# Optimization experiments

Measured on AMD Instinct MI355X. Metric: run time of the kernel, lower is better.

The kernel has to match this reference:

```python
import jax, jax.numpy as jnp
import numpy as np

NUM_HIDDENS = 1024
NUM_VOCABS = 4096
BATCH = 64
SEQ = 256


def setup_inputs() -> dict:
    key = jax.random.key(0)
    ks = jax.random.split(key, 16)
    V, H = NUM_VOCABS, NUM_HIDDENS

    def gate(k1, k2):
        return (jax.random.normal(k1, (V, H), jnp.float32) * 0.01,
                jax.random.normal(k2, (H, H), jnp.float32) * 0.01,
                jnp.zeros((H,), jnp.float32))

    f_w_xh, f_w_hh, f_b = gate(ks[0], ks[1])
    i_w_xh, i_w_hh, i_b = gate(ks[2], ks[3])
    c_w_xh, c_w_hh, c_b = gate(ks[4], ks[5])
    o_w_xh, o_w_hh, o_b = gate(ks[6], ks[7])
    y_w_ho = jax.random.normal(ks[8], (H, V), jnp.float32) * 0.01
    y_b_o = jnp.zeros((V,), jnp.float32)
    inputs = jax.random.randint(ks[9], (BATCH, SEQ), 0, V, dtype=jnp.int64)
    H0 = jnp.zeros((BATCH, H), jnp.float32)
    C0 = jnp.zeros((BATCH, H), jnp.float32)
    return dict(inputs=inputs, H0=H0, C0=C0,
                f_w_xh=f_w_xh, f_w_hh=f_w_hh, f_b=f_b,
                i_w_xh=i_w_xh, i_w_hh=i_w_hh, i_b=i_b,
                c_w_xh=c_w_xh, c_w_hh=c_w_hh, c_b=c_b,
                o_w_xh=o_w_xh, o_w_hh=o_w_hh, o_b=o_b,
                y_w_ho=y_w_ho, y_b_o=y_b_o)


def reference(inputs, H0, C0,
              f_w_xh, f_w_hh, f_b,
              i_w_xh, i_w_hh, i_b,
              c_w_xh, c_w_hh, c_b,
              o_w_xh, o_w_hh, o_b,
              y_w_ho, y_b_o):
    # inputs: (batch, seq) int tokens -> iterate over time (seq, batch)
    tokens = inputs.T  # (T, B)

    def step(carry, x_t):
        Hs, Cs = carry
        # one_hot(x) @ W_xh == gather of rows: exact same math in fp32
        f = jax.nn.sigmoid(f_w_xh[x_t] + Hs @ f_w_hh + f_b)
        i = jax.nn.sigmoid(i_w_xh[x_t] + Hs @ i_w_hh + i_b)
        o = jax.nn.sigmoid(o_w_xh[x_t] + Hs @ o_w_hh + o_b)
        C_tilde = jnp.tanh(c_w_xh[x_t] + Hs @ c_w_hh + c_b)
        Cn = f * Cs + i * C_tilde
        Hn = o * Cn  # NOTE: source applies no tanh here (faithful)
        Y = Hn @ y_w_ho + y_b_o
        return (Hn, Cn), Y

    (Hf, Cf), Ys = jax.lax.scan(step, (H0, C0), tokens)
    return Ys, Hf, Cf  # Ys: (T, B, V)
```

## Files before the change

### kernel.cpp

```cpp
#include <hip/hip_runtime.h>
#include <stdint.h>
#include <stddef.h>


#define B_ 64
#define H_ 1024
#define V_ 4096
#define T_ 256
#define NWG 128

typedef __attribute__((ext_vector_type(8))) short short8;
typedef __attribute__((ext_vector_type(4))) float f32x4;
typedef __attribute__((ext_vector_type(4))) float float4_;
typedef __attribute__((ext_vector_type(4))) unsigned int uint4v;

static __device__ __forceinline__ unsigned short f2bf(float f) {
  union { float f; unsigned int u; } v; v.f = f;
  unsigned int u = v.u;
  unsigned int r = (u + 0x7fffu + ((u >> 16) & 1u)) >> 16;
  return (unsigned short)r;
}

static __device__ __forceinline__ void gload_lds16(const void* g, void* l) {
  __builtin_amdgcn_global_load_lds((const __attribute__((address_space(1))) unsigned int*)g,
                                   (__attribute__((address_space(3))) unsigned int*)l,
                                   16, 0, 0);
}

static __device__ __forceinline__ void sc_store_u32(unsigned int* p, unsigned int v) {
  asm volatile("global_store_dword %0, %1, off sc0 sc1"
               :: "v"((unsigned long long)p), "v"(v) : "memory");
}

static __device__ __forceinline__ void pollw(const unsigned int* arr, unsigned int tgt, int lane) {
  const unsigned long long a0 = (unsigned long long)arr + (unsigned long long)lane * 16;
  const unsigned long long a1 = a0 + 1024;
  while (true) {
    uint4v v0, v1;
    asm volatile("global_load_dwordx4 %0, %2, off sc0 sc1\n\t"
                 "global_load_dwordx4 %1, %3, off sc0 sc1\n\t"
                 "s_waitcnt vmcnt(0)"
                 : "=&v"(v0), "=&v"(v1) : "v"(a0), "v"(a1) : "memory");
    const bool ok = v0[0] >= tgt && v0[1] >= tgt && v0[2] >= tgt && v0[3] >= tgt &&
                    v1[0] >= tgt && v1[1] >= tgt && v1[2] >= tgt && v1[3] >= tgt;
    if (__all(ok)) break;
  }
  asm volatile("" ::: "memory");
  __builtin_amdgcn_sched_barrier(0);
}

__global__ void transpose_bf16_kernel(const float* __restrict__ src, int src_cols,
                                      unsigned short* __restrict__ dst,
                                      int c_mul, int c_add) {
  __shared__ float tile[64][65];
  const int k0 = blockIdx.x * 64, h0 = blockIdx.y * 64;
  const int t = threadIdx.x;
  {
    const int kk = t >> 2, seg = (t & 3) * 16;
    const float* s = src + (size_t)(k0 + kk) * src_cols + h0 + seg;
#pragma unroll
    for (int j = 0; j < 16; j += 4) {
      float4_ v = *(const float4_*)(s + j);
      tile[kk][seg + j + 0] = v[0];
      tile[kk][seg + j + 1] = v[1];
      tile[kk][seg + j + 2] = v[2];
      tile[kk][seg + j + 3] = v[3];
    }
  }
  __syncthreads();
  {
    const int hh = t >> 2, ks = (t & 3) * 16;
    const int c = (h0 + hh) * c_mul + c_add;
    short8 p0, p1;
#pragma unroll
    for (int j = 0; j < 8; ++j) {
      p0[j] = (short)f2bf(tile[ks + j][hh]);
      p1[j] = (short)f2bf(tile[ks + 8 + j][hh]);
    }
    unsigned short* d = dst + (size_t)c * 1024 + k0 + ks;
    *(short8*)(d) = p0;
    *(short8*)(d + 8) = p1;
  }
}

__global__ void init_kernel(const float* __restrict__ H0,
                            unsigned short* __restrict__ Hbuf0,
                            unsigned int* __restrict__ arr) {
  const int i = blockIdx.x * 256 + threadIdx.x;
  Hbuf0[i] = f2bf(H0[i]);
  if (i < 512) sc_store_u32(arr + i, 0u);
}

#define AOFF 65536

__launch_bounds__(256, 1)
__global__ void lstm_persistent_kernel(
    const unsigned short* __restrict__ Wcat,
    unsigned short* __restrict__ Hbuf,
    unsigned int* __restrict__ arr,
    const float* __restrict__ C0,
    const float* __restrict__ xwf, const float* __restrict__ xwi,
    const float* __restrict__ xwc, const float* __restrict__ xwo,
    const float* __restrict__ bfv, const float* __restrict__ biv,
    const float* __restrict__ bcv, const float* __restrict__ bov,
    const int* __restrict__ tokens,
    float* __restrict__ outH, float* __restrict__ outC) {
  __shared__ __align__(16) unsigned char lds[147456];
  const int tid = threadIdx.x;
  const int wave = tid >> 6, lane = tid & 63;
  const int l15 = lane & 15, l4 = lane >> 4;
  const int wgc0 = blockIdx.x * 32;
  const int hbase0 = wgc0 >> 2;
  const int brow = wave * 16 + l15;
  unsigned int* myslot = arr + blockIdx.x * 4 + wave;

  auto xw_of = [&](int g) -> const float* {
    return g == 0 ? xwf : g == 1 ? xwi : g == 2 ? xwc : xwo;
  };
  auto b_of = [&](int g) -> const float* {
    return g == 0 ? bfv : g == 1 ? biv : g == 2 ? bcv : bov;
  };

  int hL[2];
  float bias8[2][4], Creg[2], xg[2][4], xgn[2][4];
#pragma unroll
  for (int ni = 0; ni < 2; ++ni) {
    hL[ni] = hbase0 + ni * 4 + l4;
#pragma unroll
    for (int r = 0; r < 4; ++r) bias8[ni][r] = b_of(r)[hL[ni]];
    Creg[ni] = C0[(size_t)brow * 1024 + hL[ni]];
  }
  {
    const int tk = tokens[brow * T_ + 0];
#pragma unroll
    for (int ni = 0; ni < 2; ++ni)
#pragma unroll
      for (int r = 0; r < 4; ++r)
        xg[ni][r] = xw_of(r)[(size_t)tk * 1024 + hL[ni]];
  }

  {
    const char* Wb = (const char*)(Wcat + (size_t)wgc0 * 1024);
#pragma unroll
    for (int it = 0; it < 16; ++it) {
      const int D = it * 4096 + wave * 1024 + lane * 16;
      const int row = D >> 11, off = D & 2047;
      const int so = off ^ ((row & 7) << 4);
      gload_lds16(Wb + (size_t)row * 2048 + so, &lds[it * 4096 + wave * 1024]);
    }
  }
  asm volatile("s_waitcnt vmcnt(0)" ::: "memory");
  __syncthreads();

  auto stageA = [&](int buf, int c, const char* Hsrc) {
#pragma unroll
    for (int it2 = 0; it2 < 4; ++it2) {
      const int row = wave * 16 + it2 * 4 + l4;
      const int so = (l15 * 16) ^ ((row & 7) << 4);
      gload_lds16(Hsrc + (size_t)row * 2048 + c * 256 + so,
                  &lds[AOFF + buf * 16384 + wave * 4096 + it2 * 1024]);
    }
  };

  const int bswz = (l15 & 7) << 4;
  f32x4 acc[2];
  const f32x4 zz = {0.f, 0.f, 0.f, 0.f};

#pragma unroll 1
  for (int t = 0; t < T_; ++t) {
    if (t > 0) pollw(arr, (unsigned int)t, lane);

    const char* Hs = (const char*)(Hbuf + (size_t)t * 65536);
    stageA(0, 0, Hs);
    stageA(1, 1, Hs);
    stageA(2, 2, Hs);
    stageA(3, 3, Hs);

    __builtin_amdgcn_sched_barrier(0);
    int tok2 = tokens[brow * T_ + ((t + 1) & (T_ - 1))];
    __builtin_amdgcn_sched_barrier(0);

    acc[0] = zz; acc[1] = zz;
#pragma unroll
    for (int c = 0; c < 8; ++c) {
      if (c < 4)       asm volatile("s_waitcnt vmcnt(13)" ::: "memory");
      else if (c == 4) asm volatile("s_waitcnt vmcnt(12)" ::: "memory");
      else if (c == 5) asm volatile("s_waitcnt vmcnt(8)" ::: "memory");
      else if (c == 6) asm volatile("s_waitcnt vmcnt(4)" ::: "memory");
      else             asm volatile("s_waitcnt vmcnt(0)" ::: "memory");
      __builtin_amdgcn_sched_barrier(0);
      if (c < 4) stageA((c + 4) % 5, c + 4, Hs);
      __builtin_amdgcn_sched_barrier(0);
      {
        const int abase = AOFF + (c % 5) * 16384;
        const int abyte = abase + brow * 256;
        const int aswz = (brow & 7) << 4;
#pragma unroll
        for (int ks = 0; ks < 4; ++ks) {
          const int koff = ks * 64 + l4 * 16;
          short8 a  = *(const short8*)&lds[abyte + (koff ^ aswz)];
          short8 b0 = *(const short8*)&lds[(size_t)l15 * 2048 + ((c * 256 + koff) ^ bswz)];
          short8 b1 = *(const short8*)&lds[(size_t)(16 + l15) * 2048 + ((c * 256 + koff) ^ bswz)];
          acc[0] = __builtin_amdgcn_mfma_f32_16x16x32_bf16(b0, a, acc[0], 0, 0, 0);
          acc[1] = __builtin_amdgcn_mfma_f32_16x16x32_bf16(b1, a, acc[1], 0, 0, 0);
        }
      }
      __builtin_amdgcn_sched_barrier(0);
    }

    if (t > 0) {
#pragma unroll
      for (int ni = 0; ni < 2; ++ni)
#pragma unroll
        for (int r = 0; r < 4; ++r) xg[ni][r] = xgn[ni][r];
    }

    unsigned short* Hout = Hbuf + (size_t)(t + 1) * 65536;
    unsigned int dat32[2][2];
#pragma unroll
    for (int ni = 0; ni < 2; ++ni) {
      const f32x4 v = acc[ni];
      const float pre0 = v[0] + xg[ni][0] + bias8[ni][0];
      const float pre1 = v[1] + xg[ni][1] + bias8[ni][1];
      const float pre2 = v[2] + xg[ni][2] + bias8[ni][2];
      const float pre3 = v[3] + xg[ni][3] + bias8[ni][3];
      const float pf = 1.f / (1.f + __expf(-pre0));
      const float pi = 1.f / (1.f + __expf(-pre1));
      const float e2 = __expf(2.f * pre2);
      const float pc = (e2 - 1.f) / (e2 + 1.f);
      const float po = 1.f / (1.f + __expf(-pre3));
      const float cn = pf * Creg[ni] + pi * pc;
      Creg[ni] = cn;
      const float hv = po * cn;
      const unsigned int sbf = f2bf(hv);
      const unsigned int p = sbf | (((unsigned int)__shfl_down(sbf, 16)) << 16);
      dat32[ni][0] = p;
      dat32[ni][1] = __shfl_down(p, 32);
      if (t == T_ - 1) {
        const size_t idx = (size_t)brow * 1024 + hL[ni];
        outH[idx] = hv; outC[idx] = cn;
      }
    }
    if (l4 == 0) {
      uint4v dat;
      dat.x = dat32[0][0]; dat.y = dat32[0][1];
      dat.z = dat32[1][0]; dat.w = dat32[1][1];
      const unsigned long long addr =
          (unsigned long long)(Hout + (size_t)brow * 1024 + hbase0);
      asm volatile("global_store_dwordx4 %0, %1, off sc0 sc1"
                   :: "v"(addr), "v"(dat) : "memory");
    }

    if (t < T_ - 1) {
      asm volatile("s_waitcnt vmcnt(0)" ::: "memory");
      if (lane == 0) sc_store_u32(myslot, (unsigned int)(t + 1));

#pragma unroll
      for (int ni = 0; ni < 2; ++ni)
#pragma unroll
        for (int r = 0; r < 4; ++r)
          xgn[ni][r] = xw_of(r)[(size_t)tok2 * 1024 + hL[ni]];
    }
  }
}

__launch_bounds__(256, 1)
__global__ void out_gemm_kernel(const unsigned short* __restrict__ A,
                                const unsigned short* __restrict__ Bw,
                                const float* __restrict__ bias,
                                float* __restrict__ Yout) {
  __shared__ unsigned char Ash[2][8192];
  __shared__ unsigned char Bsh[2][8192];
  const int tid = threadIdx.x;
  const int wave = tid >> 6, lane = tid & 63;
  const int wm = wave >> 1, wn = wave & 1;
  const int bid = blockIdx.x;
  const int tn = bid & 31, tm = bid >> 5;

  const char* Agb = (const char*)(A + (size_t)tm * 128 * 1024);
  const char* Bgb = (const char*)(Bw + (size_t)tn * 128 * 1024);

  f32x4 acc[4][4];
  const f32x4 zz = {0.f, 0.f, 0.f, 0.f};
#pragma unroll
  for (int mi = 0; mi < 4; ++mi)
#pragma unroll
    for (int ni = 0; ni < 4; ++ni) acc[mi][ni] = zz;

  auto stage = [&](int buf, int kc) {
#pragma unroll
    for (int j = 0; j < 2; ++j) {
      const int wbase = wave * 2048 + j * 1024;
      const int D = wbase + lane * 16;
      const int row = D >> 6, off = D & 63;
      const int so = off ^ ((row & 3) << 4);
      gload_lds16(Agb + (size_t)row * 2048 + kc * 64 + so, &Ash[buf][wbase]);
      gload_lds16(Bgb + (size_t)row * 2048 + kc * 64 + so, &Bsh[buf][wbase]);
    }
  };

  stage(0, 0);
  __syncthreads();

#pragma unroll 1
  for (int kc = 0; kc < 32; ++kc) {
    const int cur = kc & 1;
    if (kc < 31) stage(cur ^ 1, kc + 1);
    short8 a[4], b[4];
#pragma unroll
    for (int mi = 0; mi < 4; ++mi) {
      const int row = wm * 64 + mi * 16 + (lane & 15);
      const int off = ((lane >> 4) * 16) ^ ((row & 3) << 4);
      a[mi] = *(const short8*)&Ash[cur][row * 64 + off];
    }
#pragma unroll
    for (int ni = 0; ni < 4; ++ni) {
      const int row = wn * 64 + ni * 16 + (lane & 15);
      const int off = ((lane >> 4) * 16) ^ ((row & 3) << 4);
      b[ni] = *(const short8*)&Bsh[cur][row * 64 + off];
    }
#pragma unroll
    for (int mi = 0; mi < 4; ++mi)
#pragma unroll
      for (int ni = 0; ni < 4; ++ni)
        acc[mi][ni] = __builtin_amdgcn_mfma_f32_16x16x32_bf16(a[mi], b[ni], acc[mi][ni], 0, 0, 0);
    __syncthreads();
  }

  const int l15 = lane & 15, l4 = lane >> 4;
#pragma unroll
  for (int ni = 0; ni < 4; ++ni) {
    const int n = tn * 128 + wn * 64 + ni * 16 + l15;
    const float bv = bias[n];
#pragma unroll
    for (int mi = 0; mi < 4; ++mi) {
#pragma unroll
      for (int r = 0; r < 4; ++r) {
        const int m = tm * 128 + wm * 64 + mi * 16 + l4 * 4 + r;
        Yout[(size_t)m * 4096 + n] = acc[mi][ni][r] + bv;
      }
    }
  }
}

extern "C" void kernel_launch(void* const* d_in, const int* in_sizes, int n_in,
                              void* d_out, int out_size, void* d_ws, size_t ws_size,
                              hipStream_t stream) {
  const int* tokens   = (const int*)d_in[0];
  const float* H0     = (const float*)d_in[1];
  const float* C0     = (const float*)d_in[2];
  const float* f_w_xh = (const float*)d_in[3];
  const float* f_w_hh = (const float*)d_in[4];
  const float* f_b    = (const float*)d_in[5];
  const float* i_w_xh = (const float*)d_in[6];
  const float* i_w_hh = (const float*)d_in[7];
  const float* i_b    = (const float*)d_in[8];
  const float* c_w_xh = (const float*)d_in[9];
  const float* c_w_hh = (const float*)d_in[10];
  const float* c_b    = (const float*)d_in[11];
  const float* o_w_xh = (const float*)d_in[12];
  const float* o_w_hh = (const float*)d_in[13];
  const float* o_b    = (const float*)d_in[14];
  const float* y_w_ho = (const float*)d_in[15];
  const float* y_b_o  = (const float*)d_in[16];

  char* ws = (char*)d_ws;
  unsigned short* Wcat = (unsigned short*)ws;
  unsigned short* ywT  = (unsigned short*)(ws + (size_t)(8u << 20));
  unsigned short* Hbuf = (unsigned short*)(ws + (size_t)(16u << 20));
  unsigned int* arr = (unsigned int*)(ws + (size_t)(16u << 20) + (size_t)257 * 65536 * 2);
  const size_t needed = (size_t)(16u << 20) + (size_t)257 * 65536 * 2 + 2048;
  if (ws_size < needed) return;

  const dim3 thr(256);
  hipLaunchKernelGGL(transpose_bf16_kernel, dim3(16, 16), thr, 0, stream, f_w_hh, 1024, Wcat, 4, 0);
  hipLaunchKernelGGL(transpose_bf16_kernel, dim3(16, 16), thr, 0, stream, i_w_hh, 1024, Wcat, 4, 1);
  hipLaunchKernelGGL(transpose_bf16_kernel, dim3(16, 16), thr, 0, stream, c_w_hh, 1024, Wcat, 4, 2);
  hipLaunchKernelGGL(transpose_bf16_kernel, dim3(16, 16), thr, 0, stream, o_w_hh, 1024, Wcat, 4, 3);
  hipLaunchKernelGGL(transpose_bf16_kernel, dim3(16, 64), thr, 0, stream, y_w_ho, 4096, ywT, 1, 0);
  hipLaunchKernelGGL(init_kernel, dim3(256), thr, 0, stream, H0, Hbuf, arr);

  float* outH = (float*)d_out + (size_t)T_ * B_ * V_;
  hipLaunchKernelGGL(lstm_persistent_kernel, dim3(NWG), thr, 0, stream,
                     Wcat, Hbuf, arr, C0,
                     f_w_xh, i_w_xh, c_w_xh, o_w_xh,
                     f_b, i_b, c_b, o_b,
                     tokens, outH, outH + 65536);

  hipLaunchKernelGGL(out_gemm_kernel, dim3(4096), thr, 0, stream,
                     Hbuf + 65536, ywT, y_b_o, (float*)d_out);
}
```

Before: 1.347 ms.

## Shrink barrier flags to u16, pipeline polling, fuse prep kernels, swizzle GEMM blocks

Sync flags shrink from 32-bit to 16-bit so one dwordx4 load per lane covers all 512 flags, and the poll loop keeps a second load in flight while it checks the first. The x-gather loads move to just after staging the H tile so they overlap the recurrent matmul (vmcnt thresholds adjusted). Five transpose launches and the init launch are merged into one prep kernel, and the output GEMM block order is remapped for better cache locality. Together these target barrier latency in the serial timestep loop and launch overhead, with the risk of extra outstanding-load pressure and a wrong vmcnt count.

```diff
diff --git a/kernel.cpp b/kernel.cpp
--- a/kernel.cpp
+++ b/kernel.cpp
@@ -27,34 +27,62 @@
                                    16, 0, 0);
 }
 
-static __device__ __forceinline__ void sc_store_u32(unsigned int* p, unsigned int v) {
-  asm volatile("global_store_dword %0, %1, off sc0 sc1"
+static __device__ __forceinline__ void sc_store_u16(unsigned short* p, unsigned int v) {
+  asm volatile("global_store_short %0, %1, off sc0 sc1"
                :: "v"((unsigned long long)p), "v"(v) : "memory");
 }
 
-static __device__ __forceinline__ void pollw(const unsigned int* arr, unsigned int tgt, int lane) {
-  const unsigned long long a0 = (unsigned long long)arr + (unsigned long long)lane * 16;
-  const unsigned long long a1 = a0 + 1024;
+static __device__ __forceinline__ bool ok8(const uint4v& v, unsigned int tgt) {
+  return (v[0] & 0xffffu) >= tgt && (v[0] >> 16) >= tgt &&
+         (v[1] & 0xffffu) >= tgt && (v[1] >> 16) >= tgt &&
+         (v[2] & 0xffffu) >= tgt && (v[2] >> 16) >= tgt &&
+         (v[3] & 0xffffu) >= tgt && (v[3] >> 16) >= tgt;
+}
+
+static __device__ __forceinline__ void pollw16(const unsigned short* arr, unsigned int tgt,
+                                               int lane, uint4v& v0, uint4v& v1) {
+  const unsigned long long a = (unsigned long long)arr + (unsigned long long)lane * 16u;
+  asm volatile("global_load_dwordx4 %0, %1, off sc0 sc1" : "=&v"(v0) : "v"(a) : "memory");
   while (true) {
-    uint4v v0, v1;
-    asm volatile("global_load_dwordx4 %0, %2, off sc0 sc1\n\t"
-                 "global_load_dwordx4 %1, %3, off sc0 sc1\n\t"
-                 "s_waitcnt vmcnt(0)"
-                 : "=&v"(v0), "=&v"(v1) : "v"(a0), "v"(a1) : "memory");
-    const bool ok = v0[0] >= tgt && v0[1] >= tgt && v0[2] >= tgt && v0[3] >= tgt &&
-                    v1[0] >= tgt && v1[1] >= tgt && v1[2] >= tgt && v1[3] >= tgt;
-    if (__all(ok)) break;
+    asm volatile("global_load_dwordx4 %0, %1, off sc0 sc1\n\ts_waitcnt vmcnt(1)"
+                 : "=&v"(v1) : "v"(a) : "memory");
+    if (__all(ok8(v0, tgt))) break;
+    asm volatile("global_load_dwordx4 %0, %1, off sc0 sc1\n\ts_waitcnt vmcnt(1)"
+                 : "=&v"(v0) : "v"(a) : "memory");
+    if (__all(ok8(v1, tgt))) break;
   }
   asm volatile("" ::: "memory");
   __builtin_amdgcn_sched_barrier(0);
 }
 
-__global__ void transpose_bf16_kernel(const float* __restrict__ src, int src_cols,
-                                      unsigned short* __restrict__ dst,
-                                      int c_mul, int c_add) {
+__global__ void prep_kernel(const float* __restrict__ f_w_hh, const float* __restrict__ i_w_hh,
+                            const float* __restrict__ c_w_hh, const float* __restrict__ o_w_hh,
+                            const float* __restrict__ y_w_ho,
+                            unsigned short* __restrict__ Wcat, unsigned short* __restrict__ ywT,
+                            const float* __restrict__ H0, unsigned short* __restrict__ Hbuf0,
+                            unsigned short* __restrict__ arr) {
+  const int z = blockIdx.z;
+  const int t = threadIdx.x;
+  if (z == 5) {
+    const int b = blockIdx.y * 16 + blockIdx.x;
+    if (b < 256) {
+      const int i = b * 256 + t;
+      Hbuf0[i] = f2bf(H0[i]);
+    } else if (b == 256 && t < 512) {
+      sc_store_u16(arr + t, 0u);
+    }
+    return;
+  }
+  const float* src; unsigned short* dst; int src_cols, c_mul, c_add;
+  if (z < 4) {
+    if (blockIdx.y >= 16) return;
+    src = (z == 0) ? f_w_hh : (z == 1) ? i_w_hh : (z == 2) ? c_w_hh : o_w_hh;
+    dst = Wcat; src_cols = 1024; c_mul = 4; c_add = z;
+  } else {
+    src = y_w_ho; dst = ywT; src_cols = 4096; c_mul = 1; c_add = 0;
+  }
   __shared__ float tile[64][65];
   const int k0 = blockIdx.x * 64, h0 = blockIdx.y * 64;
-  const int t = threadIdx.x;
   {
     const int kk = t >> 2, seg = (t & 3) * 16;
     const float* s = src + (size_t)(k0 + kk) * src_cols + h0 + seg;
@@ -83,21 +111,13 @@
   }
 }
 
-__global__ void init_kernel(const float* __restrict__ H0,
-                            unsigned short* __restrict__ Hbuf0,
-                            unsigned int* __restrict__ arr) {
-  const int i = blockIdx.x * 256 + threadIdx.x;
-  Hbuf0[i] = f2bf(H0[i]);
-  if (i < 512) sc_store_u32(arr + i, 0u);
-}
-
 #define AOFF 65536
 
 __launch_bounds__(256, 1)
 __global__ void lstm_persistent_kernel(
     const unsigned short* __restrict__ Wcat,
     unsigned short* __restrict__ Hbuf,
-    unsigned int* __restrict__ arr,
+    unsigned short* __restrict__ arr,
     const float* __restrict__ C0,
     const float* __restrict__ xwf, const float* __restrict__ xwi,
     const float* __restrict__ xwc, const float* __restrict__ xwo,
@@ -112,7 +132,7 @@
   const int wgc0 = blockIdx.x * 32;
   const int hbase0 = wgc0 >> 2;
   const int brow = wave * 16 + l15;
-  unsigned int* myslot = arr + blockIdx.x * 4 + wave;
+  unsigned short* myslot = arr + blockIdx.x * 4 + wave;
 
   auto xw_of = [&](int g) -> const float* {
     return g == 0 ? xwf : g == 1 ? xwi : g == 2 ? xwc : xwo;
@@ -122,7 +142,7 @@
   };
 
   int hL[2];
-  float bias8[2][4], Creg[2], xg[2][4], xgn[2][4];
+  float bias8[2][4], Creg[2], xg[2][4];
 #pragma unroll
   for (int ni = 0; ni < 2; ++ni) {
     hL[ni] = hbase0 + ni * 4 + l4;
@@ -130,14 +150,7 @@
     for (int r = 0; r < 4; ++r) bias8[ni][r] = b_of(r)[hL[ni]];
     Creg[ni] = C0[(size_t)brow * 1024 + hL[ni]];
   }
-  {
-    const int tk = tokens[brow * T_ + 0];
-#pragma unroll
-    for (int ni = 0; ni < 2; ++ni)
-#pragma unroll
-      for (int r = 0; r < 4; ++r)
-        xg[ni][r] = xw_of(r)[(size_t)tk * 1024 + hL[ni]];
-  }
+  int tok2 = tokens[brow * T_ + 0];
 
   {
     const char* Wb = (const char*)(Wcat + (size_t)wgc0 * 1024);
@@ -165,25 +178,31 @@
   const int bswz = (l15 & 7) << 4;
   f32x4 acc[2];
   const f32x4 zz = {0.f, 0.f, 0.f, 0.f};
+  uint4v pk0 = {0, 0, 0, 0}, pk1 = {0, 0, 0, 0};
 
 #pragma unroll 1
   for (int t = 0; t < T_; ++t) {
-    if (t > 0) pollw(arr, (unsigned int)t, lane);
+    pollw16(arr, (unsigned int)t, lane, pk0, pk1);
 
     const char* Hs = (const char*)(Hbuf + (size_t)t * 65536);
     stageA(0, 0, Hs);
     stageA(1, 1, Hs);
     stageA(2, 2, Hs);
     stageA(3, 3, Hs);
-
     __builtin_amdgcn_sched_barrier(0);
-    int tok2 = tokens[brow * T_ + ((t + 1) & (T_ - 1))];
+    const int tok_next = tokens[brow * T_ + ((t + 1) & (T_ - 1))];
     __builtin_amdgcn_sched_barrier(0);
+#pragma unroll
+    for (int ni = 0; ni < 2; ++ni)
+#pragma unroll
+      for (int r = 0; r < 4; ++r)
+        xg[ni][r] = xw_of(r)[(size_t)tok2 * 1024 + hL[ni]];
+    __builtin_amdgcn_sched_barrier(0);
 
     acc[0] = zz; acc[1] = zz;
 #pragma unroll
     for (int c = 0; c < 8; ++c) {
-      if (c < 4)       asm volatile("s_waitcnt vmcnt(13)" ::: "memory");
+      if (c < 4)       asm volatile("s_waitcnt vmcnt(21)" ::: "memory");
       else if (c == 4) asm volatile("s_waitcnt vmcnt(12)" ::: "memory");
       else if (c == 5) asm volatile("s_waitcnt vmcnt(8)" ::: "memory");
       else if (c == 6) asm volatile("s_waitcnt vmcnt(4)" ::: "memory");
@@ -207,13 +226,9 @@
       }
       __builtin_amdgcn_sched_barrier(0);
     }
-
-    if (t > 0) {
-#pragma unroll
-      for (int ni = 0; ni < 2; ++ni)
-#pragma unroll
-        for (int r = 0; r < 4; ++r) xg[ni][r] = xgn[ni][r];
-    }
+    asm volatile("" :: "v"(pk0), "v"(pk1));
+
+    tok2 = tok_next;
 
     unsigned short* Hout = Hbuf + (size_t)(t + 1) * 65536;
     unsigned int dat32[2][2];
@@ -253,13 +268,7 @@
 
     if (t < T_ - 1) {
       asm volatile("s_waitcnt vmcnt(0)" ::: "memory");
-      if (lane == 0) sc_store_u32(myslot, (unsigned int)(t + 1));
-
-#pragma unroll
-      for (int ni = 0; ni < 2; ++ni)
-#pragma unroll
-        for (int r = 0; r < 4; ++r)
-          xgn[ni][r] = xw_of(r)[(size_t)tok2 * 1024 + hL[ni]];
+      if (lane == 0) sc_store_u16(myslot, (unsigned int)(t + 1));
     }
   }
 }
@@ -274,7 +283,7 @@
   const int tid = threadIdx.x;
   const int wave = tid >> 6, lane = tid & 63;
   const int wm = wave >> 1, wn = wave & 1;
-  const int bid = blockIdx.x;
+  const int bid = (blockIdx.x & 7) * 512 + (blockIdx.x >> 3);
   const int tn = bid & 31, tm = bid >> 5;
 
   const char* Agb = (const char*)(A + (size_t)tm * 128 * 1024);
@@ -368,17 +377,14 @@
   unsigned short* Wcat = (unsigned short*)ws;
   unsigned short* ywT  = (unsigned short*)(ws + (size_t)(8u << 20));
   unsigned short* Hbuf = (unsigned short*)(ws + (size_t)(16u << 20));
-  unsigned int* arr = (unsigned int*)(ws + (size_t)(16u << 20) + (size_t)257 * 65536 * 2);
-  const size_t needed = (size_t)(16u << 20) + (size_t)257 * 65536 * 2 + 2048;
+  unsigned short* arr = (unsigned short*)(ws + (size_t)(16u << 20) + (size_t)257 * 65536 * 2);
+  const size_t needed = (size_t)(16u << 20) + (size_t)257 * 65536 * 2 + 1024;
   if (ws_size < needed) return;
 
   const dim3 thr(256);
-  hipLaunchKernelGGL(transpose_bf16_kernel, dim3(16, 16), thr, 0, stream, f_w_hh, 1024, Wcat, 4, 0);
-  hipLaunchKernelGGL(transpose_bf16_kernel, dim3(16, 16), thr, 0, stream, i_w_hh, 1024, Wcat, 4, 1);
-  hipLaunchKernelGGL(transpose_bf16_kernel, dim3(16, 16), thr, 0, stream, c_w_hh, 1024, Wcat, 4, 2);
-  hipLaunchKernelGGL(transpose_bf16_kernel, dim3(16, 16), thr, 0, stream, o_w_hh, 1024, Wcat, 4, 3);
-  hipLaunchKernelGGL(transpose_bf16_kernel, dim3(16, 64), thr, 0, stream, y_w_ho, 4096, ywT, 1, 0);
-  hipLaunchKernelGGL(init_kernel, dim3(256), thr, 0, stream, H0, Hbuf, arr);
+  hipLaunchKernelGGL(prep_kernel, dim3(16, 64, 6), thr, 0, stream,
+                     f_w_hh, i_w_hh, c_w_hh, o_w_hh, y_w_ho,
+                     Wcat, ywT, H0, Hbuf, arr);
 
   float* outH = (float*)d_out + (size_t)T_ * B_ * V_;
   hipLaunchKernelGGL(lstm_persistent_kernel, dim3(NWG), thr, 0, stream,
```

New measurement: 3.234 ms. 2.4x slower.
